# Optimization experiments

Measured on AMD Instinct MI355X. Metric: run time of the kernel, lower is better.

The kernel has to match this reference:

```python
import jax, jax.numpy as jnp
import numpy as np

VOCAB, EMB, HIDDEN, OUT = 50000, 300, 512, 2
SEQ, BATCH = 512, 1024


def setup_inputs() -> dict:
    key = jax.random.key(0)
    k_text, k_len, k_emb, k_w1, k_b1, k_w2, k_b2 = jax.random.split(key, 7)
    text = jax.random.randint(k_text, (SEQ, BATCH), 1, VOCAB, dtype=jnp.int64 if jax.config.jax_enable_x64 else jnp.int32)
    lengths = jax.random.randint(k_len, (BATCH,), 1, SEQ + 1, dtype=text.dtype)
    emb_table = jax.random.normal(k_emb, (VOCAB, EMB), dtype=jnp.float32) * 0.1
    emb_table = emb_table.at[0].set(0.0)  # padding_idx=0 row zeroed like nn.Embedding
    W1 = jax.random.normal(k_w1, (EMB, HIDDEN), dtype=jnp.float32) * (1.0 / np.sqrt(EMB))
    b1 = jax.random.normal(k_b1, (HIDDEN,), dtype=jnp.float32) * 0.01
    W2 = jax.random.normal(k_w2, (HIDDEN, OUT), dtype=jnp.float32) * (1.0 / np.sqrt(HIDDEN))
    b2 = jax.random.normal(k_b2, (OUT,), dtype=jnp.float32) * 0.01
    return {"text": text, "lengths": lengths, "emb_table": emb_table,
            "W1": W1, "b1": b1, "W2": W2, "b2": b2}


def reference(text, lengths, emb_table, W1, b1, W2, b2):
    # text: [S, B] int; embedding lookup -> [S, B, E]
    embedded = emb_table[text]
    # masked mean over the first `lengths[b]` tokens (vectorized segment mean)
    seq = embedded.shape[0]
    mask = (jnp.arange(seq)[:, None] < lengths[None, :]).astype(embedded.dtype)  # [S, B]
    pooled = jnp.einsum('sbe,sb->be', embedded, mask) / lengths[:, None].astype(embedded.dtype)  # [B, E]
    # fc1 -> (dropout p=0, identity) -> relu -> fc2
    h = jax.nn.relu(pooled @ W1 + b1)
    return h @ W2 + b2
```

## Files before the change

kernel.cpp:

```cpp
#include <hip/hip_runtime.h>

typedef float f32x4 __attribute__((ext_vector_type(4)));

constexpr int EMB    = 300;
constexpr int EMB4   = 75;
constexpr int HIDDEN = 512;
constexpr int SEQ    = 512;
constexpr int BATCH  = 1024;
constexpr int VOCAB  = 50000;
constexpr int NBUK   = 32;
constexpr int BDIV   = 1563;
constexpr int NX     = 8;
constexpr int GMLP   = 8;
constexpr int NCONV  = 1792;
constexpr int ELEM4  = VOCAB * EMB / 4;

__device__ __forceinline__ unsigned short f2bf(float x) {
    unsigned u = __float_as_uint(x);
    u += 0x7fffu + ((u >> 16) & 1u);
    return (unsigned short)(u >> 16);
}

__device__ __forceinline__ f32x4 bf4up(uint2 u) {
    f32x4 r;
    r.x = __uint_as_float(u.x << 16);
    r.y = __uint_as_float(u.x & 0xffff0000u);
    r.z = __uint_as_float(u.y << 16);
    r.w = __uint_as_float(u.y & 0xffff0000u);
    return r;
}

__global__ __launch_bounds__(256) void prep_kernel(
    const int* __restrict__ text,
    const int* __restrict__ lengths,
    const float* __restrict__ emb,
    int* __restrict__ btok,
    int* __restrict__ boff,
    unsigned short* __restrict__ ebf,
    int doConv)
{
    __shared__ int4 tstage[SEQ];
    __shared__ int  hist[4][8][NBUK + 2];

    const int tid = threadIdx.x;

    if (blockIdx.x >= 256) {
        if (!doConv) return;
        const float4* src = (const float4*)emb;
        ushort4*      dst = (ushort4*)ebf;
        const int gtid = (blockIdx.x - 256) * 256 + tid;
        for (int i = gtid; i < ELEM4; i += NCONV * 256) {
            const float4 v = src[i];
            ushort4 o;
            o.x = f2bf(v.x); o.y = f2bf(v.y);
            o.z = f2bf(v.z); o.w = f2bf(v.w);
            dst[i] = o;
        }
        return;
    }

    const int wave = tid >> 6;
    const int lane = tid & 63;
    const int b0   = blockIdx.x * 4;
    const int b    = b0 + wave;
    const int len  = lengths[b];
    const unsigned long long lt = (1ull << lane) - 1ull;

    for (int s = tid; s < SEQ; s += 256)
        tstage[s] = *(const int4*)&text[(size_t)s * BATCH + b0];
    for (int i = tid; i < 4 * 8 * (NBUK + 2); i += 256)
        ((int*)hist)[i] = 0;
    __syncthreads();

    int tokv[8], kv[8], rkv[8];
#pragma unroll
    for (int c = 0; c < 8; ++c) {
        const int s      = c * 64 + lane;
        const bool valid = s < len;
        const int tok = valid ? ((const int*)&tstage[s])[wave] : 0;
        const int k   = valid ? tok / BDIV : NBUK;
        unsigned long long mm = ~0ull;
#pragma unroll
        for (int bit = 0; bit < 6; ++bit) {
            const unsigned long long bl = __ballot((k >> bit) & 1);
            mm &= ((k >> bit) & 1) ? bl : ~bl;
        }
        const int rk = __popcll(mm & lt);
        tokv[c] = tok; kv[c] = k; rkv[c] = rk;
        if (valid && rk == 0) hist[wave][c][k] = __popcll(mm);
    }
    __syncthreads();

    int tot = 0;
    if (lane < NBUK) {
#pragma unroll
        for (int c = 0; c < 8; ++c) {
            const int t = hist[wave][c][lane];
            hist[wave][c][lane] = tot;
            tot += t;
        }
    }
    int incl = tot;
#pragma unroll
    for (int off = 1; off < 32; off <<= 1) {
        const int v = __shfl_up(incl, off);
        if (lane >= off && lane < NBUK) incl += v;
    }
    const int excl = incl - tot;
    if (lane < NBUK)      boff[b * (NBUK + 1) + lane] = excl;
    if (lane == NBUK - 1) boff[b * (NBUK + 1) + NBUK] = incl;
    __syncthreads();

#pragma unroll
    for (int c = 0; c < 8; ++c) {
        const int s  = c * 64 + lane;
        const int k  = kv[c];
        const int bb = __shfl(excl, k);
        const int pos = bb + hist[wave][c][k] + rkv[c];
        if (s < len) btok[(size_t)b * SEQ + pos] = tokv[c];
    }
}

__global__ __launch_bounds__(256) void pool_kernel(
    const int* __restrict__ btok,
    const int* __restrict__ boff,
    const unsigned short* __restrict__ ebf,
    float* __restrict__ partial)
{
    __shared__ int toks[4][SEQ];

    const int wave = threadIdx.x >> 6;
    const int lane = threadIdx.x & 63;
    const int x    = blockIdx.x & (NX - 1);
    const int b    = (blockIdx.x >> 3) * 4 + wave;
    const int NJ   = NBUK / NX;

    const int lo = boff[b * (NBUK + 1) + x * NJ];
    const int hi = boff[b * (NBUK + 1) + x * NJ + NJ];
    const int n  = hi - lo;

    for (int t = lane; t < n; t += 64)
        toks[wave][t] = btok[(size_t)b * SEQ + lo + t];

    const uint2* e2 = (const uint2*)ebf;
    const bool two  = lane < (EMB4 - 64);
    const int  c2   = 64 + lane;

    f32x4 A = {0.f, 0.f, 0.f, 0.f};
    f32x4 B = A, C = A;
    int i = 0;
    for (; i + 4 <= n; i += 4) {
        const int4 t4 = *(const int4*)&toks[wave][i];
        const uint2 u0 = e2[(size_t)t4.x * EMB4 + lane];
        const uint2 u1 = e2[(size_t)t4.y * EMB4 + lane];
        const uint2 u2 = e2[(size_t)t4.z * EMB4 + lane];
        const uint2 u3 = e2[(size_t)t4.w * EMB4 + lane];
        A += bf4up(u0) + bf4up(u1);
        B += bf4up(u2) + bf4up(u3);
        if (two) {
            const uint2 w0 = e2[(size_t)t4.x * EMB4 + c2];
            const uint2 w1 = e2[(size_t)t4.y * EMB4 + c2];
            const uint2 w2 = e2[(size_t)t4.z * EMB4 + c2];
            const uint2 w3 = e2[(size_t)t4.w * EMB4 + c2];
            C += (bf4up(w0) + bf4up(w1)) + (bf4up(w2) + bf4up(w3));
        }
    }
    for (; i < n; ++i) {
        const int tk = toks[wave][i];
        A += bf4up(e2[(size_t)tk * EMB4 + lane]);
        if (two) C += bf4up(e2[(size_t)tk * EMB4 + c2]);
    }
    A += B;

    f32x4* dst = (f32x4*)(partial + ((size_t)x * BATCH + b) * EMB);
    dst[lane] = A;
    if (two) dst[c2] = C;
}

template<int NXT>
__global__ __launch_bounds__(512) void mlp_kernel(
    const float* __restrict__ partial,
    const int* __restrict__ lengths,
    const float* __restrict__ W1,
    const float* __restrict__ b1,
    const float* __restrict__ W2,
    const float* __restrict__ b2,
    float* __restrict__ out)
{
    __shared__ f32x4 pQ[GMLP / 4][EMB];
    __shared__ float hsh[GMLP][HIDDEN];

    const int b0  = blockIdx.x * GMLP;
    const int tid = threadIdx.x;

    float* pQf = (float*)pQ;
    for (int i = tid; i < EMB * GMLP; i += 512) {
        const int g = i / EMB;
        const int e = i - g * EMB;
        float s = 0.f;
#pragma unroll
        for (int xx = 0; xx < NXT; ++xx)
            s += partial[((size_t)xx * BATCH + b0 + g) * EMB + e];
        pQf[((g >> 2) * EMB + e) * 4 + (g & 3)] = s / (float)lengths[b0 + g];
    }
    __syncthreads();

    const int j = tid;
    const float bias = b1[j];
    f32x4 acc0 = {bias, bias, bias, bias};
    f32x4 acc1 = acc0;

#pragma unroll 10
    for (int e = 0; e < EMB; ++e) {
        const float w = W1[(size_t)e * HIDDEN + j];
        acc0 += pQ[0][e] * w;
        acc1 += pQ[1][e] * w;
    }
    hsh[0][j] = fmaxf(acc0.x, 0.f);
    hsh[1][j] = fmaxf(acc0.y, 0.f);
    hsh[2][j] = fmaxf(acc0.z, 0.f);
    hsh[3][j] = fmaxf(acc0.w, 0.f);
    hsh[4][j] = fmaxf(acc1.x, 0.f);
    hsh[5][j] = fmaxf(acc1.y, 0.f);
    hsh[6][j] = fmaxf(acc1.z, 0.f);
    hsh[7][j] = fmaxf(acc1.w, 0.f);
    __syncthreads();

    const int w    = tid >> 6;
    const int lane = tid & 63;
    const f32x4* W2v = (const f32x4*)W2;
    float s0 = 0.f, s1 = 0.f;
#pragma unroll
    for (int q = 0; q < 2; ++q) {
        const int cc = lane + q * 64;
        const f32x4 hv = *(const f32x4*)&hsh[w][4 * cc];
        const f32x4 wA = W2v[2 * cc + 0];
        const f32x4 wB = W2v[2 * cc + 1];
        s0 += hv.x * wA.x + hv.y * wA.z + hv.z * wB.x + hv.w * wB.z;
        s1 += hv.x * wA.y + hv.y * wA.w + hv.z * wB.y + hv.w * wB.w;
    }
#pragma unroll
    for (int off = 32; off > 0; off >>= 1) {
        s0 += __shfl_down(s0, off);
        s1 += __shfl_down(s1, off);
    }
    if (lane == 0) {
        out[(b0 + w) * 2 + 0] = s0 + b2[0];
        out[(b0 + w) * 2 + 1] = s1 + b2[1];
    }
}

__global__ __launch_bounds__(320) void naive_pool(
    const int* __restrict__ text, const int* __restrict__ lengths,
    const float* __restrict__ emb, float* __restrict__ pooled)
{
    __shared__ int toks[SEQ];
    const int b = blockIdx.x;
    const int len = lengths[b];
    for (int s = threadIdx.x; s < len; s += 320)
        toks[s] = text[(size_t)s * BATCH + b];
    __syncthreads();
    const int e = threadIdx.x;
    if (e < EMB) {
        float a = 0.f;
        for (int s = 0; s < len; ++s)
            a += emb[(size_t)toks[s] * EMB + e];
        pooled[(size_t)b * EMB + e] = a;
    }
}

extern "C" void kernel_launch(void* const* d_in, const int* in_sizes, int n_in,
                              void* d_out, int out_size, void* d_ws, size_t ws_size,
                              hipStream_t stream) {
    const int*   text    = (const int*)d_in[0];
    const int*   lengths = (const int*)d_in[1];
    const float* emb     = (const float*)d_in[2];
    const float* W1      = (const float*)d_in[3];
    const float* b1      = (const float*)d_in[4];
    const float* W2      = (const float*)d_in[5];
    const float* b2      = (const float*)d_in[6];
    float*       out     = (float*)d_out;

    char* ws = (char*)d_ws;
    const size_t btokBytes = (size_t)BATCH * SEQ * sizeof(int);
    const size_t boffBytes = (size_t)BATCH * (NBUK + 1) * sizeof(int);
    const size_t ebfBytes  = (size_t)VOCAB * EMB * sizeof(unsigned short);
    const size_t poolBytes = (size_t)BATCH * EMB * sizeof(float);

    int* btok = (int*)ws;
    int* boff = (int*)(ws + btokBytes);
    size_t off = btokBytes + boffBytes;
    off = (off + 63) & ~(size_t)63;
    unsigned short* ebf = (unsigned short*)(ws + off);
    float* partial = (float*)(ws + off + ebfBytes);

    const size_t need = off + ebfBytes + (size_t)NX * poolBytes;

    if (ws_size >= need) {
        prep_kernel<<<256 + NCONV, 256, 0, stream>>>(
            text, lengths, emb, btok, boff, ebf, 1);
        pool_kernel<<<NX * (BATCH / 4), 256, 0, stream>>>(btok, boff, ebf, partial);
        mlp_kernel<8><<<BATCH / GMLP, 512, 0, stream>>>(
            partial, lengths, W1, b1, W2, b2, out);
    } else {
        float* pooled = (float*)ws;
        naive_pool<<<BATCH, 320, 0, stream>>>(text, lengths, emb, pooled);
        mlp_kernel<1><<<BATCH / GMLP, 512, 0, stream>>>(
            pooled, lengths, W1, b1, W2, b2, out);
    }
}
```

Measured before the change: 63.40 us.

## Fuse prep, pool and MLP into one cooperative persistent kernel with grid syncs

Merges the three launches into one cooperative kernel of 2048 blocks. The bucketize/convert, pooling and MLP phases are separated by grid-wide syncs and share a union of shared-memory layouts. This is meant to remove launch gaps and kernel-boundary drains. The MLP phase is also reworked to 256 threads, with each thread computing two hidden units and fc2 folded in through wave shuffles instead of a shared hidden buffer. Risks are grid-sync overhead, the fixed 2048-block grid needing 8 blocks per CU to fit, and the per-call host queries for occupancy and device attributes.

Result: slower. 79.47 us (+25.3%).

```diff
diff --git a/kernel.cpp b/kernel.cpp
--- a/kernel.cpp
+++ b/kernel.cpp
@@ -1,4 +1,7 @@
 #include <hip/hip_runtime.h>
+#include <hip/hip_cooperative_groups.h>
+
+namespace cg = cooperative_groups;
 
 typedef float f32x4 __attribute__((ext_vector_type(4)));
 
@@ -12,8 +15,11 @@
 constexpr int BDIV   = 1563;
 constexpr int NX     = 8;
 constexpr int GMLP   = 8;
+constexpr int NBLK   = 2048;
+constexpr int NCONVF = NBLK - 256;
 constexpr int NCONV  = 1792;
 constexpr int ELEM4  = VOCAB * EMB / 4;
+constexpr int MLPB   = BATCH / GMLP;
 
 __device__ __forceinline__ unsigned short f2bf(float x) {
     unsigned u = __float_as_uint(x);
@@ -30,46 +36,35 @@
     return r;
 }
 
-__global__ __launch_bounds__(256) void prep_kernel(
-    const int* __restrict__ text,
-    const int* __restrict__ lengths,
-    const float* __restrict__ emb,
-    int* __restrict__ btok,
-    int* __restrict__ boff,
-    unsigned short* __restrict__ ebf,
-    int doConv)
-{
-    __shared__ int4 tstage[SEQ];
-    __shared__ int  hist[4][8][NBUK + 2];
-
-    const int tid = threadIdx.x;
-
-    if (blockIdx.x >= 256) {
-        if (!doConv) return;
-        const float4* src = (const float4*)emb;
-        ushort4*      dst = (ushort4*)ebf;
-        const int gtid = (blockIdx.x - 256) * 256 + tid;
-        for (int i = gtid; i < ELEM4; i += NCONV * 256) {
-            const float4 v = src[i];
-            ushort4 o;
-            o.x = f2bf(v.x); o.y = f2bf(v.y);
-            o.z = f2bf(v.z); o.w = f2bf(v.w);
-            dst[i] = o;
-        }
-        return;
-    }
-
+__device__ __forceinline__ f32x4 relu4(f32x4 v) {
+    v.x = fmaxf(v.x, 0.f); v.y = fmaxf(v.y, 0.f);
+    v.z = fmaxf(v.z, 0.f); v.w = fmaxf(v.w, 0.f);
+    return v;
+}
+
+union SharedU {
+    struct { int4 tstage[SEQ]; int hist[4][8][NBUK + 2]; } bz;
+    struct { int toks[4][SEQ]; } pool;
+    struct { f32x4 pQ[GMLP / 4][EMB]; f32x4 red[4][4]; } mlp;
+};
+
+__device__ void bucketize_phase(SharedU& sh, int bid, int tid,
+                                const int* __restrict__ text,
+                                const int* __restrict__ lengths,
+                                int* __restrict__ btok,
+                                int* __restrict__ boff)
+{
     const int wave = tid >> 6;
     const int lane = tid & 63;
-    const int b0   = blockIdx.x * 4;
+    const int b0   = bid * 4;
     const int b    = b0 + wave;
     const int len  = lengths[b];
     const unsigned long long lt = (1ull << lane) - 1ull;
 
     for (int s = tid; s < SEQ; s += 256)
-        tstage[s] = *(const int4*)&text[(size_t)s * BATCH + b0];
+        sh.bz.tstage[s] = *(const int4*)&text[(size_t)s * BATCH + b0];
     for (int i = tid; i < 4 * 8 * (NBUK + 2); i += 256)
-        ((int*)hist)[i] = 0;
+        ((int*)sh.bz.hist)[i] = 0;
     __syncthreads();
 
     int tokv[8], kv[8], rkv[8];
@@ -77,7 +72,7 @@
     for (int c = 0; c < 8; ++c) {
         const int s      = c * 64 + lane;
         const bool valid = s < len;
-        const int tok = valid ? ((const int*)&tstage[s])[wave] : 0;
+        const int tok = valid ? ((const int*)&sh.bz.tstage[s])[wave] : 0;
         const int k   = valid ? tok / BDIV : NBUK;
         unsigned long long mm = ~0ull;
 #pragma unroll
@@ -87,7 +82,7 @@
         }
         const int rk = __popcll(mm & lt);
         tokv[c] = tok; kv[c] = k; rkv[c] = rk;
-        if (valid && rk == 0) hist[wave][c][k] = __popcll(mm);
+        if (valid && rk == 0) sh.bz.hist[wave][c][k] = __popcll(mm);
     }
     __syncthreads();
 
@@ -95,8 +90,8 @@
     if (lane < NBUK) {
 #pragma unroll
         for (int c = 0; c < 8; ++c) {
-            const int t = hist[wave][c][lane];
-            hist[wave][c][lane] = tot;
+            const int t = sh.bz.hist[wave][c][lane];
+            sh.bz.hist[wave][c][lane] = tot;
             tot += t;
         }
     }
@@ -116,23 +111,21 @@
         const int s  = c * 64 + lane;
         const int k  = kv[c];
         const int bb = __shfl(excl, k);
-        const int pos = bb + hist[wave][c][k] + rkv[c];
+        const int pos = bb + sh.bz.hist[wave][c][k] + rkv[c];
         if (s < len) btok[(size_t)b * SEQ + pos] = tokv[c];
     }
 }
 
-__global__ __launch_bounds__(256) void pool_kernel(
-    const int* __restrict__ btok,
-    const int* __restrict__ boff,
-    const unsigned short* __restrict__ ebf,
-    float* __restrict__ partial)
-{
-    __shared__ int toks[4][SEQ];
-
-    const int wave = threadIdx.x >> 6;
-    const int lane = threadIdx.x & 63;
-    const int x    = blockIdx.x & (NX - 1);
-    const int b    = (blockIdx.x >> 3) * 4 + wave;
+__device__ void pool_phase(SharedU& sh, int bid, int tid,
+                           const int* __restrict__ btok,
+                           const int* __restrict__ boff,
+                           const unsigned short* __restrict__ ebf,
+                           float* __restrict__ partial)
+{
+    const int wave = tid >> 6;
+    const int lane = tid & 63;
+    const int x    = bid & (NX - 1);
+    const int b    = (bid >> 3) * 4 + wave;
     const int NJ   = NBUK / NX;
 
     const int lo = boff[b * (NBUK + 1) + x * NJ];
@@ -140,7 +133,7 @@
     const int n  = hi - lo;
 
     for (int t = lane; t < n; t += 64)
-        toks[wave][t] = btok[(size_t)b * SEQ + lo + t];
+        sh.pool.toks[wave][t] = btok[(size_t)b * SEQ + lo + t];
 
     const uint2* e2 = (const uint2*)ebf;
     const bool two  = lane < (EMB4 - 64);
@@ -150,7 +143,7 @@
     f32x4 B = A, C = A;
     int i = 0;
     for (; i + 4 <= n; i += 4) {
-        const int4 t4 = *(const int4*)&toks[wave][i];
+        const int4 t4 = *(const int4*)&sh.pool.toks[wave][i];
         const uint2 u0 = e2[(size_t)t4.x * EMB4 + lane];
         const uint2 u1 = e2[(size_t)t4.y * EMB4 + lane];
         const uint2 u2 = e2[(size_t)t4.z * EMB4 + lane];
@@ -166,7 +159,7 @@
         }
     }
     for (; i < n; ++i) {
-        const int tk = toks[wave][i];
+        const int tk = sh.pool.toks[wave][i];
         A += bf4up(e2[(size_t)tk * EMB4 + lane]);
         if (two) C += bf4up(e2[(size_t)tk * EMB4 + c2]);
     }
@@ -177,77 +170,154 @@
     if (two) dst[c2] = C;
 }
 
-template<int NXT>
-__global__ __launch_bounds__(512) void mlp_kernel(
-    const float* __restrict__ partial,
-    const int* __restrict__ lengths,
-    const float* __restrict__ W1,
-    const float* __restrict__ b1,
-    const float* __restrict__ W2,
-    const float* __restrict__ b2,
-    float* __restrict__ out)
-{
-    __shared__ f32x4 pQ[GMLP / 4][EMB];
-    __shared__ float hsh[GMLP][HIDDEN];
-
-    const int b0  = blockIdx.x * GMLP;
-    const int tid = threadIdx.x;
-
-    float* pQf = (float*)pQ;
-    for (int i = tid; i < EMB * GMLP; i += 512) {
+__device__ void mlp_phase(SharedU& sh, int bid, int tid,
+                          const float* __restrict__ partial,
+                          const int* __restrict__ lengths,
+                          const float* __restrict__ W1,
+                          const float* __restrict__ b1,
+                          const float* __restrict__ W2,
+                          const float* __restrict__ b2,
+                          float* __restrict__ out)
+{
+    const int b0 = bid * GMLP;
+
+    float* pQf = (float*)sh.mlp.pQ;
+    for (int i = tid; i < EMB * GMLP; i += 256) {
         const int g = i / EMB;
         const int e = i - g * EMB;
         float s = 0.f;
 #pragma unroll
-        for (int xx = 0; xx < NXT; ++xx)
+        for (int xx = 0; xx < NX; ++xx)
             s += partial[((size_t)xx * BATCH + b0 + g) * EMB + e];
         pQf[((g >> 2) * EMB + e) * 4 + (g & 3)] = s / (float)lengths[b0 + g];
     }
     __syncthreads();
 
-    const int j = tid;
-    const float bias = b1[j];
-    f32x4 acc0 = {bias, bias, bias, bias};
-    f32x4 acc1 = acc0;
-
-#pragma unroll 10
+    const int j0 = tid, j1 = tid + 256;
+    const float bi0 = b1[j0], bi1 = b1[j1];
+    f32x4 a00 = {bi0, bi0, bi0, bi0}, a01 = a00;
+    f32x4 a10 = {bi1, bi1, bi1, bi1}, a11 = a10;
+#pragma unroll 4
     for (int e = 0; e < EMB; ++e) {
-        const float w = W1[(size_t)e * HIDDEN + j];
-        acc0 += pQ[0][e] * w;
-        acc1 += pQ[1][e] * w;
-    }
-    hsh[0][j] = fmaxf(acc0.x, 0.f);
-    hsh[1][j] = fmaxf(acc0.y, 0.f);
-    hsh[2][j] = fmaxf(acc0.z, 0.f);
-    hsh[3][j] = fmaxf(acc0.w, 0.f);
-    hsh[4][j] = fmaxf(acc1.x, 0.f);
-    hsh[5][j] = fmaxf(acc1.y, 0.f);
-    hsh[6][j] = fmaxf(acc1.z, 0.f);
-    hsh[7][j] = fmaxf(acc1.w, 0.f);
-    __syncthreads();
-
-    const int w    = tid >> 6;
-    const int lane = tid & 63;
-    const f32x4* W2v = (const f32x4*)W2;
-    float s0 = 0.f, s1 = 0.f;
-#pragma unroll
-    for (int q = 0; q < 2; ++q) {
-        const int cc = lane + q * 64;
-        const f32x4 hv = *(const f32x4*)&hsh[w][4 * cc];
-        const f32x4 wA = W2v[2 * cc + 0];
-        const f32x4 wB = W2v[2 * cc + 1];
-        s0 += hv.x * wA.x + hv.y * wA.z + hv.z * wB.x + hv.w * wB.z;
-        s1 += hv.x * wA.y + hv.y * wA.w + hv.z * wB.y + hv.w * wB.w;
-    }
-#pragma unroll
-    for (int off = 32; off > 0; off >>= 1) {
-        s0 += __shfl_down(s0, off);
-        s1 += __shfl_down(s1, off);
-    }
-    if (lane == 0) {
-        out[(b0 + w) * 2 + 0] = s0 + b2[0];
-        out[(b0 + w) * 2 + 1] = s1 + b2[1];
-    }
+        const float w0 = W1[(size_t)e * HIDDEN + j0];
+        const float w1 = W1[(size_t)e * HIDDEN + j1];
+        const f32x4 p0 = sh.mlp.pQ[0][e];
+        const f32x4 p1 = sh.mlp.pQ[1][e];
+        a00 += p0 * w0; a01 += p1 * w0;
+        a10 += p0 * w1; a11 += p1 * w1;
+    }
+    a00 = relu4(a00); a01 = relu4(a01);
+    a10 = relu4(a10); a11 = relu4(a11);
+
+    const float w2a0 = W2[j0 * 2 + 0], w2a1 = W2[j0 * 2 + 1];
+    const float w2b0 = W2[j1 * 2 + 0], w2b1 = W2[j1 * 2 + 1];
+    f32x4 s00 = a00 * w2a0 + a10 * w2b0;
+    f32x4 s01 = a01 * w2a0 + a11 * w2b0;
+    f32x4 s10 = a00 * w2a1 + a10 * w2b1;
+    f32x4 s11 = a01 * w2a1 + a11 * w2b1;
+
+#define WRED(v)                                                     \
+    for (int o = 32; o > 0; o >>= 1) {                              \
+        v.x += __shfl_down(v.x, o); v.y += __shfl_down(v.y, o);     \
+        v.z += __shfl_down(v.z, o); v.w += __shfl_down(v.w, o);     \
+    }
+    WRED(s00) WRED(s01) WRED(s10) WRED(s11)
+#undef WRED
+
+    const int wv = tid >> 6, ln = tid & 63;
+    if (ln == 0) {
+        sh.mlp.red[wv][0] = s00; sh.mlp.red[wv][1] = s01;
+        sh.mlp.red[wv][2] = s10; sh.mlp.red[wv][3] = s11;
+    }
+    __syncthreads();
+    if (tid == 0) {
+        f32x4 t0 = sh.mlp.red[0][0] + sh.mlp.red[1][0] + sh.mlp.red[2][0] + sh.mlp.red[3][0];
+        f32x4 t1 = sh.mlp.red[0][1] + sh.mlp.red[1][1] + sh.mlp.red[2][1] + sh.mlp.red[3][1];
+        f32x4 t2 = sh.mlp.red[0][2] + sh.mlp.red[1][2] + sh.mlp.red[2][2] + sh.mlp.red[3][2];
+        f32x4 t3 = sh.mlp.red[0][3] + sh.mlp.red[1][3] + sh.mlp.red[2][3] + sh.mlp.red[3][3];
+        const float z0 = b2[0], z1 = b2[1];
+        out[(b0 + 0) * 2 + 0] = t0.x + z0; out[(b0 + 0) * 2 + 1] = t2.x + z1;
+        out[(b0 + 1) * 2 + 0] = t0.y + z0; out[(b0 + 1) * 2 + 1] = t2.y + z1;
+        out[(b0 + 2) * 2 + 0] = t0.z + z0; out[(b0 + 2) * 2 + 1] = t2.z + z1;
+        out[(b0 + 3) * 2 + 0] = t0.w + z0; out[(b0 + 3) * 2 + 1] = t2.w + z1;
+        out[(b0 + 4) * 2 + 0] = t1.x + z0; out[(b0 + 4) * 2 + 1] = t3.x + z1;
+        out[(b0 + 5) * 2 + 0] = t1.y + z0; out[(b0 + 5) * 2 + 1] = t3.y + z1;
+        out[(b0 + 6) * 2 + 0] = t1.z + z0; out[(b0 + 6) * 2 + 1] = t3.z + z1;
+        out[(b0 + 7) * 2 + 0] = t1.w + z0; out[(b0 + 7) * 2 + 1] = t3.w + z1;
+    }
+}
+
+__global__ __launch_bounds__(256, 8) void fused_kernel(
+    const int* text, const int* lengths, const float* emb,
+    const float* W1, const float* b1, const float* W2, const float* b2,
+    float* out, int* btok, int* boff, unsigned short* ebf, float* partial)
+{
+    __shared__ SharedU sh;
+    const int bid = blockIdx.x;
+    const int tid = threadIdx.x;
+
+    if (bid < 256) {
+        bucketize_phase(sh, bid, tid, text, lengths, btok, boff);
+    } else {
+        const float4* src = (const float4*)emb;
+        ushort4*      dst = (ushort4*)ebf;
+        const int gtid = (bid - 256) * 256 + tid;
+        for (int i = gtid; i < ELEM4; i += NCONVF * 256) {
+            const float4 v = src[i];
+            ushort4 o;
+            o.x = f2bf(v.x); o.y = f2bf(v.y);
+            o.z = f2bf(v.z); o.w = f2bf(v.w);
+            dst[i] = o;
+        }
+    }
+    cg::this_grid().sync();
+
+    pool_phase(sh, bid, tid, btok, boff, ebf, partial);
+    cg::this_grid().sync();
+
+    if (bid < MLPB)
+        mlp_phase(sh, bid, tid, partial, lengths, W1, b1, W2, b2, out);
+}
+
+__global__ __launch_bounds__(256) void prep_kernel(
+    const int* __restrict__ text, const int* __restrict__ lengths,
+    const float* __restrict__ emb, int* __restrict__ btok,
+    int* __restrict__ boff, unsigned short* __restrict__ ebf)
+{
+    __shared__ SharedU sh;
+    const int tid = threadIdx.x;
+    if (blockIdx.x >= 256) {
+        const float4* src = (const float4*)emb;
+        ushort4*      dst = (ushort4*)ebf;
+        const int gtid = (blockIdx.x - 256) * 256 + tid;
+        for (int i = gtid; i < ELEM4; i += NCONV * 256) {
+            const float4 v = src[i];
+            ushort4 o;
+            o.x = f2bf(v.x); o.y = f2bf(v.y);
+            o.z = f2bf(v.z); o.w = f2bf(v.w);
+            dst[i] = o;
+        }
+        return;
+    }
+    bucketize_phase(sh, blockIdx.x, tid, text, lengths, btok, boff);
+}
+
+__global__ __launch_bounds__(256) void pool_kernel(
+    const int* __restrict__ btok, const int* __restrict__ boff,
+    const unsigned short* __restrict__ ebf, float* __restrict__ partial)
+{
+    __shared__ SharedU sh;
+    pool_phase(sh, blockIdx.x, threadIdx.x, btok, boff, ebf, partial);
+}
+
+__global__ __launch_bounds__(256) void mlp_kernel(
+    const float* __restrict__ partial, const int* __restrict__ lengths,
+    const float* __restrict__ W1, const float* __restrict__ b1,
+    const float* __restrict__ W2, const float* __restrict__ b2,
+    float* __restrict__ out)
+{
+    __shared__ SharedU sh;
+    mlp_phase(sh, blockIdx.x, threadIdx.x, partial, lengths, W1, b1, W2, b2, out);
 }
 
 __global__ __launch_bounds__(320) void naive_pool(
@@ -266,6 +336,74 @@
         for (int s = 0; s < len; ++s)
             a += emb[(size_t)toks[s] * EMB + e];
         pooled[(size_t)b * EMB + e] = a;
+    }
+}
+
+__global__ __launch_bounds__(256) void mlp1_kernel(
+    const float* __restrict__ pooled, const int* __restrict__ lengths,
+    const float* __restrict__ W1, const float* __restrict__ b1,
+    const float* __restrict__ W2, const float* __restrict__ b2,
+    float* __restrict__ out)
+{
+    __shared__ SharedU sh;
+    const int b0  = blockIdx.x * GMLP;
+    const int tid = threadIdx.x;
+    float* pQf = (float*)sh.mlp.pQ;
+    for (int i = tid; i < EMB * GMLP; i += 256) {
+        const int g = i / EMB;
+        const int e = i - g * EMB;
+        pQf[((g >> 2) * EMB + e) * 4 + (g & 3)] =
+            pooled[(size_t)(b0 + g) * EMB + e] / (float)lengths[b0 + g];
+    }
+    __syncthreads();
+    const int j0 = tid, j1 = tid + 256;
+    const float bi0 = b1[j0], bi1 = b1[j1];
+    f32x4 a00 = {bi0, bi0, bi0, bi0}, a01 = a00;
+    f32x4 a10 = {bi1, bi1, bi1, bi1}, a11 = a10;
+#pragma unroll 4
+    for (int e = 0; e < EMB; ++e) {
+        const float w0 = W1[(size_t)e * HIDDEN + j0];
+        const float w1 = W1[(size_t)e * HIDDEN + j1];
+        const f32x4 p0 = sh.mlp.pQ[0][e];
+        const f32x4 p1 = sh.mlp.pQ[1][e];
+        a00 += p0 * w0; a01 += p1 * w0;
+        a10 += p0 * w1; a11 += p1 * w1;
+    }
+    a00 = relu4(a00); a01 = relu4(a01);
+    a10 = relu4(a10); a11 = relu4(a11);
+    const float w2a0 = W2[j0 * 2 + 0], w2a1 = W2[j0 * 2 + 1];
+    const float w2b0 = W2[j1 * 2 + 0], w2b1 = W2[j1 * 2 + 1];
+    f32x4 s00 = a00 * w2a0 + a10 * w2b0;
+    f32x4 s01 = a01 * w2a0 + a11 * w2b0;
+    f32x4 s10 = a00 * w2a1 + a10 * w2b1;
+    f32x4 s11 = a01 * w2a1 + a11 * w2b1;
+#define WRED(v)                                                     \
+    for (int o = 32; o > 0; o >>= 1) {                              \
+        v.x += __shfl_down(v.x, o); v.y += __shfl_down(v.y, o);     \
+        v.z += __shfl_down(v.z, o); v.w += __shfl_down(v.w, o);     \
+    }
+    WRED(s00) WRED(s01) WRED(s10) WRED(s11)
+#undef WRED
+    const int wv = tid >> 6, ln = tid & 63;
+    if (ln == 0) {
+        sh.mlp.red[wv][0] = s00; sh.mlp.red[wv][1] = s01;
+        sh.mlp.red[wv][2] = s10; sh.mlp.red[wv][3] = s11;
+    }
+    __syncthreads();
+    if (tid == 0) {
+        f32x4 t0 = sh.mlp.red[0][0] + sh.mlp.red[1][0] + sh.mlp.red[2][0] + sh.mlp.red[3][0];
+        f32x4 t1 = sh.mlp.red[0][1] + sh.mlp.red[1][1] + sh.mlp.red[2][1] + sh.mlp.red[3][1];
+        f32x4 t2 = sh.mlp.red[0][2] + sh.mlp.red[1][2] + sh.mlp.red[2][2] + sh.mlp.red[3][2];
+        f32x4 t3 = sh.mlp.red[0][3] + sh.mlp.red[1][3] + sh.mlp.red[2][3] + sh.mlp.red[3][3];
+        const float z0 = b2[0], z1 = b2[1];
+        out[(b0 + 0) * 2 + 0] = t0.x + z0; out[(b0 + 0) * 2 + 1] = t2.x + z1;
+        out[(b0 + 1) * 2 + 0] = t0.y + z0; out[(b0 + 1) * 2 + 1] = t2.y + z1;
+        out[(b0 + 2) * 2 + 0] = t0.z + z0; out[(b0 + 2) * 2 + 1] = t2.z + z1;
+        out[(b0 + 3) * 2 + 0] = t0.w + z0; out[(b0 + 3) * 2 + 1] = t2.w + z1;
+        out[(b0 + 4) * 2 + 0] = t1.x + z0; out[(b0 + 4) * 2 + 1] = t3.x + z1;
+        out[(b0 + 5) * 2 + 0] = t1.y + z0; out[(b0 + 5) * 2 + 1] = t3.y + z1;
+        out[(b0 + 6) * 2 + 0] = t1.z + z0; out[(b0 + 6) * 2 + 1] = t3.z + z1;
+        out[(b0 + 7) * 2 + 0] = t1.w + z0; out[(b0 + 7) * 2 + 1] = t3.w + z1;
     }
 }
 
@@ -290,22 +428,35 @@
     int* btok = (int*)ws;
     int* boff = (int*)(ws + btokBytes);
     size_t off = btokBytes + boffBytes;
-    off = (off + 63) & ~(size_t)63;
+    off = (off + 127) & ~(size_t)127;
     unsigned short* ebf = (unsigned short*)(ws + off);
     float* partial = (float*)(ws + off + ebfBytes);
-
     const size_t need = off + ebfBytes + (size_t)NX * poolBytes;
 
-    if (ws_size >= need) {
-        prep_kernel<<<256 + NCONV, 256, 0, stream>>>(
-            text, lengths, emb, btok, boff, ebf, 1);
-        pool_kernel<<<NX * (BATCH / 4), 256, 0, stream>>>(btok, boff, ebf, partial);
-        mlp_kernel<8><<<BATCH / GMLP, 512, 0, stream>>>(
-            partial, lengths, W1, b1, W2, b2, out);
-    } else {
+    if (ws_size < need) {
         float* pooled = (float*)ws;
         naive_pool<<<BATCH, 320, 0, stream>>>(text, lengths, emb, pooled);
-        mlp_kernel<1><<<BATCH / GMLP, 512, 0, stream>>>(
-            pooled, lengths, W1, b1, W2, b2, out);
-    }
-}
+        mlp1_kernel<<<BATCH / GMLP, 256, 0, stream>>>(pooled, lengths, W1, b1, W2, b2, out);
+        return;
+    }
+
+    int dev = 0;
+    hipGetDevice(&dev);
+    int coop = 0, nCU = 0, maxb = 0;
+    hipDeviceGetAttribute(&coop, hipDeviceAttributeCooperativeLaunch, dev);
+    hipDeviceGetAttribute(&nCU, hipDeviceAttributeMultiprocessorCount, dev);
+    hipOccupancyMaxActiveBlocksPerMultiprocessor(&maxb, fused_kernel, 256, 0);
+
+    if (coop && (long)maxb * nCU >= NBLK) {
+        void* args[] = {(void*)&text, (void*)&lengths, (void*)&emb,
+                        (void*)&W1, (void*)&b1, (void*)&W2, (void*)&b2,
+                        (void*)&out, (void*)&btok, (void*)&boff,
+                        (void*)&ebf, (void*)&partial};
+        hipLaunchCooperativeKernel((void*)fused_kernel, dim3(NBLK), dim3(256),
+                                   args, 0, stream);
+    } else {
+        prep_kernel<<<256 + NCONV, 256, 0, stream>>>(text, lengths, emb, btok, boff, ebf);
+        pool_kernel<<<NX * (BATCH / 4), 256, 0, stream>>>(btok, boff, ebf, partial);
+        mlp_kernel<<<MLPB, 256, 0, stream>>>(partial, lengths, W1, b1, W2, b2, out);
+    }
+}
```
